# Kernel tuning notes

Measured on AMD Instinct MI355X. Metric: run time of the kernel, lower is better.

The kernel has to match this reference:

```python
import jax, jax.numpy as jnp
import numpy as np
import math
from jax import lax

B, L = 64, 8192
S = L // 8          # width after 3 stride-(1,2) SAME convs
D = 4 * 5           # height(4) * channels(5) -> per-token feature dim
D_FLAT = S * D


def setup_inputs():
    key = jax.random.key(0)
    ks = jax.random.split(key, 32)
    sc = 0.1
    inp = {
        "inputs": jax.random.randint(ks[0], (B, L), 0, 4, dtype=jnp.int32),
        # conv stack: HWIO kernels, Conv2D(5,(4,4),(1,2),'SAME')
        "conv_w1": sc * jax.random.normal(ks[1], (4, 4, 1, 5), jnp.float32),
        "conv_b1": jnp.zeros((5,), jnp.float32),
        "conv_w2": sc * jax.random.normal(ks[2], (4, 4, 5, 5), jnp.float32),
        "conv_b2": jnp.zeros((5,), jnp.float32),
        "conv_w3": sc * jax.random.normal(ks[3], (4, 4, 5, 5), jnp.float32),
        "conv_b3": jnp.zeros((5,), jnp.float32),
        # 3 SelfAttn blocks, each with K/Q/V projections [D, D]
        "attn1_K": sc * jax.random.normal(ks[4], (D, D), jnp.float32),
        "attn1_Q": sc * jax.random.normal(ks[5], (D, D), jnp.float32),
        "attn1_V": sc * jax.random.normal(ks[6], (D, D), jnp.float32),
        "attn2_K": sc * jax.random.normal(ks[7], (D, D), jnp.float32),
        "attn2_Q": sc * jax.random.normal(ks[8], (D, D), jnp.float32),
        "attn2_V": sc * jax.random.normal(ks[9], (D, D), jnp.float32),
        "attn3_K": sc * jax.random.normal(ks[10], (D, D), jnp.float32),
        "attn3_Q": sc * jax.random.normal(ks[11], (D, D), jnp.float32),
        "attn3_V": sc * jax.random.normal(ks[12], (D, D), jnp.float32),
        # 3 Dense(10) layers (no activation, as in Keras defaults)
        "dense_w1": 0.01 * jax.random.normal(ks[13], (D_FLAT, 10), jnp.float32),
        "dense_b1": jnp.zeros((10,), jnp.float32),
        "dense_w2": sc * jax.random.normal(ks[14], (10, 10), jnp.float32),
        "dense_b2": jnp.zeros((10,), jnp.float32),
        "dense_w3": sc * jax.random.normal(ks[15], (10, 10), jnp.float32),
        "dense_b3": jnp.zeros((10,), jnp.float32),
    }
    return inp


def _conv(x, w, b):
    # NHWC, HWIO, strides (1,2), SAME
    y = lax.conv_general_dilated(x, w, window_strides=(1, 2), padding="SAME",
                                 dimension_numbers=("NHWC", "HWIO", "NHWC"))
    return y + b


def _self_attn(x, Kw, Qw, Vw):
    # x: [B, S, D]; manual causal scaled dot-product attention
    K = x @ Kw
    Q = x @ Qw
    V = x @ Vw
    s = Q.shape[1]
    mask = jnp.triu(jnp.full((s, s), -jnp.inf, dtype=x.dtype), k=1)
    scores = jnp.einsum("bsd,btd->bst", Q, K) / math.sqrt(K.shape[-1]) + mask
    return jax.nn.softmax(scores, axis=-1) @ V


def reference(inputs, conv_w1, conv_b1, conv_w2, conv_b2, conv_w3, conv_b3,
              attn1_K, attn1_Q, attn1_V, attn2_K, attn2_Q, attn2_V,
              attn3_K, attn3_Q, attn3_V,
              dense_w1, dense_b1, dense_w2, dense_b2, dense_w3, dense_b3):
    # one_hot over axis=1 -> [B, 4, L], then channel dim -> [B, 4, L, 1]
    x = jax.nn.one_hot(inputs, 4, axis=1, dtype=jnp.float32)[..., None]
    x = _conv(x, conv_w1, conv_b1)
    x = _conv(x, conv_w2, conv_b2)
    x = _conv(x, conv_w3, conv_b3)            # [B, 4, S, 5]
    # tokens along width, features = height(4) x channels(5)
    x = jnp.transpose(x, (0, 2, 1, 3)).reshape(x.shape[0], S, D)
    x = _self_attn(x, attn1_K, attn1_Q, attn1_V)
    x = _self_attn(x, attn2_K, attn2_Q, attn2_V)
    x = _self_attn(x, attn3_K, attn3_Q, attn3_V)
    x = x.reshape(x.shape[0], -1)             # flatten [B, S*D]
    x = x @ dense_w1 + dense_b1
    x = x @ dense_w2 + dense_b2
    x = x @ dense_w3 + dense_b3               # [B, 10]
    return x
```

## Files before the change

### kernel.cpp

```cpp
#include <hip/hip_runtime.h>
#include <hip/hip_bf16.h>


#define B_ 64
#define L_ 8192
#define S_ 1024
#define D_ 20

typedef unsigned short ushort_t;
typedef __attribute__((ext_vector_type(8))) short short8_t;
typedef __attribute__((ext_vector_type(4))) short short4_t;
typedef __attribute__((ext_vector_type(4))) float f32x4_t;

__device__ __forceinline__ ushort_t f2bf(float f) {
  unsigned u = __float_as_uint(f);
  return (ushort_t)((u + 0x7fffu + ((u >> 16) & 1u)) >> 16);
}
__device__ __forceinline__ float bf2f(ushort_t h) {
  return __uint_as_float(((unsigned)h) << 16);
}

__global__ __launch_bounds__(256) void conv12_kernel(
    const int* __restrict__ inp,
    const float* __restrict__ W1c, const float* __restrict__ B1c,
    const float* __restrict__ W2c, const float* __restrict__ B2c,
    float* __restrict__ out,
    const float* __restrict__ W1d,
    float* __restrict__ W1T) {
  __shared__ float w1s[80], b1s[5], w2s[400], b2s[5];
  for (int j = threadIdx.x; j < 400; j += 256) w2s[j] = W2c[j];
  if (threadIdx.x < 80)      w1s[threadIdx.x]      = W1c[threadIdx.x];
  else if (threadIdx.x < 85) b1s[threadIdx.x - 80] = B1c[threadIdx.x - 80];
  else if (threadIdx.x < 90) b2s[threadIdx.x - 85] = B2c[threadIdx.x - 85];
  __syncthreads();
  const int idx = blockIdx.x * 256 + threadIdx.x;
  const int b  = idx >> 11;
  const int wo = idx & 2047;
  const int* ib = inp + (size_t)b * L_;
  int iv[10];
#pragma unroll
  for (int t = 0; t < 10; ++t) {
    int g = 4 * wo - 3 + t;
    iv[t] = (g >= 0 && g < L_) ? ib[g] : -100;
  }
  float val[4][4][5];
#pragma unroll
  for (int pos = 0; pos < 4; ++pos) {
    const int w1 = 2 * wo - 1 + pos;
    const bool okp = (w1 >= 0 && w1 < 4096);
#pragma unroll
    for (int hi = 0; hi < 4; ++hi)
#pragma unroll
      for (int ci = 0; ci < 5; ++ci) val[hi][pos][ci] = okp ? b1s[ci] : 0.f;
    if (okp) {
#pragma unroll
      for (int kw = 0; kw < 4; ++kw) {
        const int gw = 2 * w1 - 1 + kw;
        if (gw >= 0 && gw < L_) {
          const int v = iv[2 * pos + kw];
#pragma unroll
          for (int hi = 0; hi < 4; ++hi) {
            const int kh = v - hi + 1;
            if (kh >= 0 && kh < 4) {
#pragma unroll
              for (int ci = 0; ci < 5; ++ci)
                val[hi][pos][ci] += w1s[(kh * 4 + kw) * 5 + ci];
            }
          }
        }
      }
    }
  }
  float acc[4][5];
#pragma unroll
  for (int h = 0; h < 4; ++h)
#pragma unroll
    for (int c = 0; c < 5; ++c) acc[h][c] = b2s[c];
#pragma unroll
  for (int kh = 0; kh < 4; ++kh)
#pragma unroll
    for (int kw = 0; kw < 4; ++kw)
#pragma unroll
      for (int ci = 0; ci < 5; ++ci) {
        const float* wp = w2s + ((kh * 4 + kw) * 5 + ci) * 5;
        float w0 = wp[0], w1v = wp[1], w2v = wp[2], w3 = wp[3], w4 = wp[4];
#pragma unroll
        for (int h = 0; h < 4; ++h) {
          int hi = h - 1 + kh;
          if (hi >= 0 && hi < 4) {
            float x = val[hi][kw][ci];
            acc[h][0] += w0 * x;  acc[h][1] += w1v * x; acc[h][2] += w2v * x;
            acc[h][3] += w3 * x;  acc[h][4] += w4 * x;
          }
        }
      }
  float* ob = out + (size_t)b * 4 * 2048 * 5;
#pragma unroll
  for (int h = 0; h < 4; ++h)
#pragma unroll
    for (int c = 0; c < 5; ++c) ob[(h * 2048 + wo) * 5 + c] = acc[h][c];
  for (int j = idx; j < 204800; j += 131072) {
    int col = j / 20480, i2 = j - col * 20480;
    W1T[j] = W1d[i2 * 10 + col];
  }
}

__global__ __launch_bounds__(256) void conv3_proj_kernel(
    const float* __restrict__ in,
    const float* __restrict__ W,  const float* __restrict__ Bi,
    const float* __restrict__ Kw, const float* __restrict__ Qw,
    const float* __restrict__ Vw,
    ushort_t* __restrict__ Qb, ushort_t* __restrict__ Kb,
    ushort_t* __restrict__ Vt) {
  constexpr int WIN = 2048;
  __shared__ float ws[400], bs[5];
  __shared__ float kw[400], qw[400], vw[400];
  for (int j = threadIdx.x; j < 400; j += 256) {
    ws[j] = W[j]; kw[j] = Kw[j]; qw[j] = Qw[j]; vw[j] = Vw[j];
  }
  if (threadIdx.x < 5) bs[threadIdx.x] = Bi[threadIdx.x];
  __syncthreads();
  const int r  = blockIdx.x * 256 + threadIdx.x;
  const int b  = r >> 10;
  const int wo = r & 1023;
  float val[4][4][5];
#pragma unroll
  for (int hi = 0; hi < 4; ++hi) {
    const float* ir = in + ((size_t)b * 4 + hi) * WIN * 5;
#pragma unroll
    for (int kwp = 0; kwp < 4; ++kwp) {
      int wi = 2 * wo - 1 + kwp;
      bool ok = (wi >= 0 && wi < WIN);
#pragma unroll
      for (int ci = 0; ci < 5; ++ci) val[hi][kwp][ci] = ok ? ir[wi * 5 + ci] : 0.f;
    }
  }
  float acc[4][5];
#pragma unroll
  for (int h = 0; h < 4; ++h)
#pragma unroll
    for (int c = 0; c < 5; ++c) acc[h][c] = bs[c];
#pragma unroll
  for (int kh = 0; kh < 4; ++kh)
#pragma unroll
    for (int kwp = 0; kwp < 4; ++kwp)
#pragma unroll
      for (int ci = 0; ci < 5; ++ci) {
        const float* wp = ws + ((kh * 4 + kwp) * 5 + ci) * 5;
        float w0 = wp[0], w1 = wp[1], w2 = wp[2], w3 = wp[3], w4 = wp[4];
#pragma unroll
        for (int h = 0; h < 4; ++h) {
          int hi = h - 1 + kh;
          if (hi >= 0 && hi < 4) {
            float x = val[hi][kwp][ci];
            acc[h][0] += w0 * x; acc[h][1] += w1 * x; acc[h][2] += w2 * x;
            acc[h][3] += w3 * x; acc[h][4] += w4 * x;
          }
        }
      }
  float x[D_];
#pragma unroll
  for (int h = 0; h < 4; ++h)
#pragma unroll
    for (int c = 0; c < 5; ++c) x[h * 5 + c] = acc[h][c];
  float q[D_], k[D_], v[D_];
#pragma unroll
  for (int j = 0; j < D_; ++j) { q[j] = 0.f; k[j] = 0.f; v[j] = 0.f; }
#pragma unroll
  for (int i = 0; i < D_; ++i) {
#pragma unroll
    for (int j = 0; j < D_; ++j) {
      q[j] += x[i] * qw[i * D_ + j];
      k[j] += x[i] * kw[i * D_ + j];
      v[j] += x[i] * vw[i * D_ + j];
    }
  }
  const float sc = 0.22360679774997896f;
  ushort_t qt[32], kt[32];
#pragma unroll
  for (int j = 0; j < D_; ++j) { qt[j] = f2bf(q[j] * sc); kt[j] = f2bf(k[j]); }
#pragma unroll
  for (int j = D_; j < 32; ++j) { qt[j] = 0; kt[j] = 0; }
  int4* qd = (int4*)(Qb + (size_t)r * 32);
  int4* kd = (int4*)(Kb + (size_t)r * 32);
#pragma unroll
  for (int j = 0; j < 4; ++j) {
    qd[j] = *(const int4*)(qt + 8 * j);
    kd[j] = *(const int4*)(kt + 8 * j);
  }
  ushort_t* vbase = Vt + ((size_t)b * 32) * 1024 + wo;
#pragma unroll
  for (int d = 0; d < D_; ++d) vbase[d * 1024] = f2bf(v[d]);
}

template <bool FUSE>
__global__ __launch_bounds__(512, 6) void attn_kernel(
    const ushort_t* __restrict__ Qb, const ushort_t* __restrict__ Kb,
    const ushort_t* __restrict__ Vt,
    const float* __restrict__ Kw2, const float* __restrict__ Qw2,
    const float* __restrict__ Vw2,
    ushort_t* __restrict__ Qb2, ushort_t* __restrict__ Kb2,
    ushort_t* __restrict__ Vt2,
    const float* __restrict__ W1T,
    float* __restrict__ part2) {
  constexpr int VST = 1032;
  __shared__ ushort_t vts[20 * VST];
  __shared__ float extraf[FUSE ? 2480 : 1280];
  __shared__ float mrgL[64];
  __shared__ float red2[FUSE ? 4 : 40];
  const int blk   = blockIdx.x;
  const int b     = blk & 63;
  const int strip = 15 - (blk >> 6);
  const int q0    = strip * 64;
  const int nt    = q0 + 64;
  const int tid   = threadIdx.x;
  const int w     = tid >> 6;
  const int sub   = w & 3;
  const int half  = w >> 2;
  const int lane  = tid & 63;
  const int n     = lane & 15;
  const int quad  = lane >> 4;
  const int qbase = q0 + 16 * sub;
  const int qg    = qbase + n;
  const ushort_t* VtB = Vt + (size_t)b * 32 * 1024;
  const int ntc = nt >> 3;
  for (int i = tid; i < 20 * ntc; i += 512) {
    int row = i / ntc, cc = i - row * ntc;
    *(int4*)(vts + row * VST + cc * 8) =
        *(const int4*)(VtB + (size_t)row * 1024 + cc * 8);
  }
  if (FUSE) {
    for (int j = tid; j < 1200; j += 512) {
      int m = j / 400, oo = j - m * 400;
      extraf[j] = (m == 0) ? Kw2[oo] : (m == 1) ? Qw2[oo] : Vw2[oo];
    }
  }
  const ushort_t* KbB = Kb + (size_t)b * 1024 * 32;
  short8_t qfrag = *(const short8_t*)(Qb + ((size_t)(b * 1024 + qbase + n)) * 32 + quad * 8);
  f32x4_t oA = {0.f, 0.f, 0.f, 0.f};
  f32x4_t oB = {0.f, 0.f, 0.f, 0.f};
  const f32x4_t zero = {0.f, 0.f, 0.f, 0.f};
  float lsum = 0.f;
  const int nt2 = nt >> 1;
  const int tlo = half ? nt2 : 0;
  int thi = half ? nt : nt2;
  if (thi > qbase + 16) thi = qbase + 16;
  __syncthreads();
  for (int t0 = tlo; t0 < thi; t0 += 32) {
    short8_t kf0 = *(const short8_t*)(KbB + (size_t)(t0 + n) * 32 + quad * 8);
    short8_t kf1 = *(const short8_t*)(KbB + (size_t)(t0 + 16 + n) * 32 + quad * 8);
#pragma unroll
    for (int c = 0; c < 2; ++c) {
      const int tg = t0 + c * 16 + quad * 4;
      f32x4_t s = __builtin_amdgcn_mfma_f32_16x16x32_bf16(c ? kf1 : kf0, qfrag,
                                                          zero, 0, 0, 0);
      ushort_t pk4[4];
#pragma unroll
      for (int r = 0; r < 4; ++r) {
        float p = (tg + r <= qg) ? __expf(s[r]) : 0.f;
        ushort_t h = f2bf(p);
        lsum += bf2f(h);
        pk4[r] = h;
      }
      short4_t pfrag = *(const short4_t*)pk4;
      short4_t vlo = *(const short4_t*)(vts + n * VST + t0 + c * 16 + quad * 4);
      short4_t vhi = *(const short4_t*)(vts + (16 + (n & 3)) * VST + t0 + c * 16 + quad * 4);
      oA = __builtin_amdgcn_mfma_f32_16x16x16bf16_1k(vlo, pfrag, oA, 0, 0, 0);
      oB = __builtin_amdgcn_mfma_f32_16x16x16bf16_1k(vhi, pfrag, oB, 0, 0, 0);
    }
  }
  float l = lsum;
  l += __shfl_xor(l, 16, 64);
  l += __shfl_xor(l, 32, 64);
  float* ox  = FUSE ? (extraf + 1200) : extraf;
  float* oxw = ox + sub * 320;
  if (half) {
#pragma unroll
    for (int r = 0; r < 4; ++r) oxw[n * 20 + quad * 4 + r] = oA[r];
    if (quad == 0) {
#pragma unroll
      for (int r = 0; r < 4; ++r) oxw[n * 20 + 16 + r] = oB[r];
      mrgL[sub * 16 + n] = l;
    }
  }
  __syncthreads();
  if (!half) {
#pragma unroll
    for (int r = 0; r < 4; ++r) oA[r] += oxw[n * 20 + quad * 4 + r];
    if (quad == 0) {
#pragma unroll
      for (int r = 0; r < 4; ++r) oB[r] += oxw[n * 20 + 16 + r];
    }
    l += mrgL[sub * 16 + n];
    const float inv = 1.f / l;
#pragma unroll
    for (int r = 0; r < 4; ++r) oxw[n * 20 + quad * 4 + r] = oA[r] * inv;
    if (quad == 0) {
#pragma unroll
      for (int r = 0; r < 4; ++r) oxw[n * 20 + 16 + r] = oB[r] * inv;
    }
  }
  if (FUSE) {
    if (!half) {
      float* pw = extraf;
      __asm__ volatile("s_waitcnt lgkmcnt(0)" ::: "memory");
      const int row  = lane >> 2;
      const int part = lane & 3;
      float x[D_];
#pragma unroll
      for (int i = 0; i < D_; ++i) x[i] = oxw[row * 20 + i];
      float qv[5], kv[5], vv[5];
#pragma unroll
      for (int jj = 0; jj < 5; ++jj) { qv[jj] = 0.f; kv[jj] = 0.f; vv[jj] = 0.f; }
#pragma unroll
      for (int i = 0; i < D_; ++i) {
        const float xi = x[i];
#pragma unroll
        for (int jj = 0; jj < 5; ++jj) {
          const int j = 5 * part + jj;
          kv[jj] += xi * pw[i * 20 + j];
          qv[jj] += xi * pw[400 + i * 20 + j];
          vv[jj] += xi * pw[800 + i * 20 + j];
        }
      }
      const float sc = 0.22360679774997896f;
      const int rg = b * 1024 + qbase + row;
      const int s  = rg & 1023;
#pragma unroll
      for (int jj = 0; jj < 5; ++jj) {
        const int j = 5 * part + jj;
        Kb2[(size_t)rg * 32 + j] = f2bf(kv[jj]);
        Qb2[(size_t)rg * 32 + j] = f2bf(qv[jj] * sc);
        Vt2[(size_t)b * 32768 + (size_t)j * 1024 + s] = f2bf(vv[jj]);
      }
      if (part == 0) {
#pragma unroll
        for (int u = 0; u < 6; ++u)
          *(unsigned*)(Kb2 + (size_t)rg * 32 + 20 + 2 * u) = 0u;
      } else if (part == 1) {
#pragma unroll
        for (int u = 0; u < 6; ++u)
          *(unsigned*)(Qb2 + (size_t)rg * 32 + 20 + 2 * u) = 0u;
      }
    }
  } else {
    __syncthreads();
    float acc[10];
#pragma unroll
    for (int j = 0; j < 10; ++j) acc[j] = 0.f;
    const int base = q0 * 20;
    if (tid < 256) {
#pragma unroll
      for (int k = 0; k < 5; ++k) {
        const int il = tid + 256 * k;
        const float xv = ox[il];
#pragma unroll
        for (int j = 0; j < 10; ++j)
          acc[j] += xv * W1T[(size_t)j * 20480 + base + il];
      }
    }
#pragma unroll
    for (int off = 1; off < 64; off <<= 1) {
#pragma unroll
      for (int j = 0; j < 10; ++j) acc[j] += __shfl_xor(acc[j], off, 64);
    }
    if (tid < 256 && lane == 0) {
#pragma unroll
      for (int j = 0; j < 10; ++j) red2[w * 10 + j] = acc[j];
    }
    __syncthreads();
    if (tid < 10) {
      float s2 = red2[tid] + red2[10 + tid] + red2[20 + tid] + red2[30 + tid];
      part2[((b << 4) + strip) * 10 + tid] = s2;
    }
  }
}

__global__ __launch_bounds__(64) void dense_final(
    const float* __restrict__ part2,
    const float* __restrict__ B1,
    const float* __restrict__ W2, const float* __restrict__ B2,
    const float* __restrict__ W3, const float* __restrict__ B3,
    float* __restrict__ out) {
  const int b = blockIdx.x;
  __shared__ float y1[10], y2[10];
  if (threadIdx.x < 10) {
    int j = threadIdx.x;
    float s = 0.f;
#pragma unroll
    for (int st = 0; st < 16; ++st) s += part2[((b << 4) + st) * 10 + j];
    y1[j] = s + B1[j];
  }
  __syncthreads();
  if (threadIdx.x < 10) {
    int j = threadIdx.x;
    float s = B2[j];
#pragma unroll
    for (int i = 0; i < 10; ++i) s += y1[i] * W2[i * 10 + j];
    y2[j] = s;
  }
  __syncthreads();
  if (threadIdx.x < 10) {
    int j = threadIdx.x;
    float s = B3[j];
#pragma unroll
    for (int i = 0; i < 10; ++i) s += y2[i] * W3[i * 10 + j];
    out[b * 10 + j] = s;
  }
}

extern "C" void kernel_launch(void* const* d_in, const int* in_sizes, int n_in,
                              void* d_out, int out_size, void* d_ws, size_t ws_size,
                              hipStream_t stream) {
  const int*   inp = (const int*)d_in[0];
  const float* cw1 = (const float*)d_in[1];
  const float* cb1 = (const float*)d_in[2];
  const float* cw2 = (const float*)d_in[3];
  const float* cb2 = (const float*)d_in[4];
  const float* cw3 = (const float*)d_in[5];
  const float* cb3 = (const float*)d_in[6];
  const float* a1K = (const float*)d_in[7];
  const float* a1Q = (const float*)d_in[8];
  const float* a1V = (const float*)d_in[9];
  const float* a2K = (const float*)d_in[10];
  const float* a2Q = (const float*)d_in[11];
  const float* a2V = (const float*)d_in[12];
  const float* a3K = (const float*)d_in[13];
  const float* a3Q = (const float*)d_in[14];
  const float* a3V = (const float*)d_in[15];
  const float* dw1 = (const float*)d_in[16];
  const float* db1 = (const float*)d_in[17];
  const float* dw2 = (const float*)d_in[18];
  const float* db2 = (const float*)d_in[19];
  const float* dw3 = (const float*)d_in[20];
  const float* db3 = (const float*)d_in[21];
  float* outp = (float*)d_out;

  float* wsf = (float*)d_ws;
  ushort_t* qbA  = (ushort_t*)(wsf);
  ushort_t* kbA  = (ushort_t*)(wsf + 1048576);
  ushort_t* vtA  = (ushort_t*)(wsf + 2097152);
  float*    part2= wsf + 4456448;
  float*    w1t  = wsf + 4466688;
  ushort_t* qbB  = (ushort_t*)(wsf + 4671488);
  ushort_t* kbB  = (ushort_t*)(wsf + 5712384);
  ushort_t* vtB  = (ushort_t*)(wsf + 6760960);
  float*    c2   = wsf + 5242880;

  conv12_kernel<<<512, 256, 0, stream>>>(inp, cw1, cb1, cw2, cb2, c2, dw1, w1t);

  conv3_proj_kernel<<<256, 256, 0, stream>>>(c2, cw3, cb3, a1K, a1Q, a1V, qbA, kbA, vtA);
  attn_kernel<true><<<1024, 512, 0, stream>>>(
      qbA, kbA, vtA, a2K, a2Q, a2V, qbB, kbB, vtB, nullptr, nullptr);
  attn_kernel<true><<<1024, 512, 0, stream>>>(
      qbB, kbB, vtB, a3K, a3Q, a3V, qbA, kbA, vtA, nullptr, nullptr);
  attn_kernel<false><<<1024, 512, 0, stream>>>(
      qbA, kbA, vtA, nullptr, nullptr, nullptr, nullptr, nullptr, nullptr,
      w1t, part2);

  dense_final<<<64, 64, 0, stream>>>(part2, db1, dw2, db2, dw3, db3, outp);
}
```

Before: 198.5 us.

## Shrink attention LDS footprint, read V high rows from global, interleave strips

The attention kernel now stages only 16 V-transpose rows in LDS and reads the remaining four rows straight from global memory. The output scratch area reuses the V buffer after an added barrier, and the launch-bounds occupancy target goes from 6 to 8 blocks. Causal strips are also assigned to blocks in an interleaved order to balance work across dispatch. The smaller LDS footprint is meant to allow more resident blocks per CU, at the cost of extra global loads in the inner loop, an additional __syncthreads, and possible register pressure from the tighter launch bound.

```diff
diff --git a/kernel.cpp b/kernel.cpp
--- a/kernel.cpp
+++ b/kernel.cpp
@@ -194,7 +194,7 @@
 }
 
 template <bool FUSE>
-__global__ __launch_bounds__(512, 6) void attn_kernel(
+__global__ __launch_bounds__(512, 8) void attn_kernel(
     const ushort_t* __restrict__ Qb, const ushort_t* __restrict__ Kb,
     const ushort_t* __restrict__ Vt,
     const float* __restrict__ Kw2, const float* __restrict__ Qw2,
@@ -204,13 +204,17 @@
     const float* __restrict__ W1T,
     float* __restrict__ part2) {
   constexpr int VST = 1032;
-  __shared__ ushort_t vts[20 * VST];
-  __shared__ float extraf[FUSE ? 2480 : 1280];
+  __shared__ __align__(16) ushort_t vts[16 * VST];
+  __shared__ float pw_s[FUSE ? 1200 : 4];
   __shared__ float mrgL[64];
-  __shared__ float red2[FUSE ? 4 : 40];
+  __shared__ float red2[40];
+  float* ox = (float*)vts;
   const int blk   = blockIdx.x;
   const int b     = blk & 63;
-  const int strip = 15 - (blk >> 6);
+  const int raw   = blk >> 6;
+  const int rr4   = raw & 3, k4 = raw >> 2;
+  const int strip = (k4 == 0) ? rr4 : (k4 == 1) ? 7 - rr4
+                  : (k4 == 2) ? 8 + rr4 : 15 - rr4;
   const int q0    = strip * 64;
   const int nt    = q0 + 64;
   const int tid   = threadIdx.x;
@@ -223,19 +227,21 @@
   const int qbase = q0 + 16 * sub;
   const int qg    = qbase + n;
   const ushort_t* VtB = Vt + (size_t)b * 32 * 1024;
-  const int ntc = nt >> 3;
-  for (int i = tid; i < 20 * ntc; i += 512) {
-    int row = i / ntc, cc = i - row * ntc;
-    *(int4*)(vts + row * VST + cc * 8) =
-        *(const int4*)(VtB + (size_t)row * 1024 + cc * 8);
+  {
+    const int row = tid >> 5, c0 = tid & 31;
+    const int ntc = nt >> 3;
+    for (int cc = c0; cc < ntc; cc += 32)
+      *(int4*)(vts + row * VST + cc * 8) =
+          *(const int4*)(VtB + (size_t)row * 1024 + cc * 8);
   }
   if (FUSE) {
     for (int j = tid; j < 1200; j += 512) {
       int m = j / 400, oo = j - m * 400;
-      extraf[j] = (m == 0) ? Kw2[oo] : (m == 1) ? Qw2[oo] : Vw2[oo];
-    }
-  }
-  const ushort_t* KbB = Kb + (size_t)b * 1024 * 32;
+      pw_s[j] = (m == 0) ? Kw2[oo] : (m == 1) ? Qw2[oo] : Vw2[oo];
+    }
+  }
+  const ushort_t* KbB  = Kb + (size_t)b * 1024 * 32;
+  const ushort_t* VtHi = VtB + (size_t)(16 + (n & 3)) * 1024;
   short8_t qfrag = *(const short8_t*)(Qb + ((size_t)(b * 1024 + qbase + n)) * 32 + quad * 8);
   f32x4_t oA = {0.f, 0.f, 0.f, 0.f};
   f32x4_t oB = {0.f, 0.f, 0.f, 0.f};
@@ -264,7 +270,7 @@
       }
       short4_t pfrag = *(const short4_t*)pk4;
       short4_t vlo = *(const short4_t*)(vts + n * VST + t0 + c * 16 + quad * 4);
-      short4_t vhi = *(const short4_t*)(vts + (16 + (n & 3)) * VST + t0 + c * 16 + quad * 4);
+      short4_t vhi = *(const short4_t*)(VtHi + t0 + c * 16 + quad * 4);
       oA = __builtin_amdgcn_mfma_f32_16x16x16bf16_1k(vlo, pfrag, oA, 0, 0, 0);
       oB = __builtin_amdgcn_mfma_f32_16x16x16bf16_1k(vhi, pfrag, oB, 0, 0, 0);
     }
@@ -272,7 +278,7 @@
   float l = lsum;
   l += __shfl_xor(l, 16, 64);
   l += __shfl_xor(l, 32, 64);
-  float* ox  = FUSE ? (extraf + 1200) : extraf;
+  __syncthreads();
   float* oxw = ox + sub * 320;
   if (half) {
 #pragma unroll
@@ -302,7 +308,6 @@
   }
   if (FUSE) {
     if (!half) {
-      float* pw = extraf;
       __asm__ volatile("s_waitcnt lgkmcnt(0)" ::: "memory");
       const int row  = lane >> 2;
       const int part = lane & 3;
@@ -318,9 +323,9 @@
 #pragma unroll
         for (int jj = 0; jj < 5; ++jj) {
           const int j = 5 * part + jj;
-          kv[jj] += xi * pw[i * 20 + j];
-          qv[jj] += xi * pw[400 + i * 20 + j];
-          vv[jj] += xi * pw[800 + i * 20 + j];
+          kv[jj] += xi * pw_s[i * 20 + j];
+          qv[jj] += xi * pw_s[400 + i * 20 + j];
+          vv[jj] += xi * pw_s[800 + i * 20 + j];
         }
       }
       const float sc = 0.22360679774997896f;
```

New measurement: 223.3 us. 12.5% more time.

## Fold dense layers 2-3 into W1 and bias, drop final dense kernel

Applied to the files above, without the earlier changes.

Because the three dense layers have no activation, W1·W2·W3 is precomputed into the transposed weight buffer and the combined bias is written straight into the output. The last attention kernel then atomically adds its per-strip partial sums into the output, and the separate dense_final launch goes away. This removes one kernel launch and the partial-sum buffer. The cost is extra per-element work in conv12 to compute W2·W3, and floating-point atomics that make the summation order nondeterministic.

```diff
diff --git a/kernel.cpp b/kernel.cpp
--- a/kernel.cpp
+++ b/kernel.cpp
@@ -26,7 +26,11 @@
     const float* __restrict__ W2c, const float* __restrict__ B2c,
     float* __restrict__ out,
     const float* __restrict__ W1d,
-    float* __restrict__ W1T) {
+    float* __restrict__ W1T,
+    const float* __restrict__ B1d, const float* __restrict__ W2d,
+    const float* __restrict__ B2d, const float* __restrict__ W3d,
+    const float* __restrict__ B3d,
+    float* __restrict__ outp) {
   __shared__ float w1s[80], b1s[5], w2s[400], b2s[5];
   for (int j = threadIdx.x; j < 400; j += 256) w2s[j] = W2c[j];
   if (threadIdx.x < 80)      w1s[threadIdx.x]      = W1c[threadIdx.x];
@@ -100,8 +104,33 @@
 #pragma unroll
     for (int c = 0; c < 5; ++c) ob[(h * 2048 + wo) * 5 + c] = acc[h][c];
   for (int j = idx; j < 204800; j += 131072) {
-    int col = j / 20480, i2 = j - col * 20480;
-    W1T[j] = W1d[i2 * 10 + col];
+    const int col = j / 20480, i2 = j - col * 20480;
+    float w23[10];
+#pragma unroll
+    for (int k2 = 0; k2 < 10; ++k2) {
+      float s = 0.f;
+#pragma unroll
+      for (int m = 0; m < 10; ++m) s += W2d[k2 * 10 + m] * W3d[m * 10 + col];
+      w23[k2] = s;
+    }
+    float s = 0.f;
+#pragma unroll
+    for (int k2 = 0; k2 < 10; ++k2) s += W1d[i2 * 10 + k2] * w23[k2];
+    W1T[j] = s;
+  }
+  if (idx < 640) {
+    const int col = idx - (idx / 10) * 10;
+    float bc = B3d[col];
+#pragma unroll
+    for (int m = 0; m < 10; ++m) bc += B2d[m] * W3d[m * 10 + col];
+#pragma unroll
+    for (int k2 = 0; k2 < 10; ++k2) {
+      float w23 = 0.f;
+#pragma unroll
+      for (int m = 0; m < 10; ++m) w23 += W2d[k2 * 10 + m] * W3d[m * 10 + col];
+      bc += B1d[k2] * w23;
+    }
+    outp[idx] = bc;
   }
 }
 
@@ -202,7 +231,7 @@
     ushort_t* __restrict__ Qb2, ushort_t* __restrict__ Kb2,
     ushort_t* __restrict__ Vt2,
     const float* __restrict__ W1T,
-    float* __restrict__ part2) {
+    float* __restrict__ outp) {
   constexpr int VST = 1032;
   __shared__ ushort_t vts[20 * VST];
   __shared__ float extraf[FUSE ? 2480 : 1280];
@@ -371,41 +400,8 @@
     __syncthreads();
     if (tid < 10) {
       float s2 = red2[tid] + red2[10 + tid] + red2[20 + tid] + red2[30 + tid];
-      part2[((b << 4) + strip) * 10 + tid] = s2;
-    }
-  }
-}
-
-__global__ __launch_bounds__(64) void dense_final(
-    const float* __restrict__ part2,
-    const float* __restrict__ B1,
-    const float* __restrict__ W2, const float* __restrict__ B2,
-    const float* __restrict__ W3, const float* __restrict__ B3,
-    float* __restrict__ out) {
-  const int b = blockIdx.x;
-  __shared__ float y1[10], y2[10];
-  if (threadIdx.x < 10) {
-    int j = threadIdx.x;
-    float s = 0.f;
-#pragma unroll
-    for (int st = 0; st < 16; ++st) s += part2[((b << 4) + st) * 10 + j];
-    y1[j] = s + B1[j];
-  }
-  __syncthreads();
-  if (threadIdx.x < 10) {
-    int j = threadIdx.x;
-    float s = B2[j];
-#pragma unroll
-    for (int i = 0; i < 10; ++i) s += y1[i] * W2[i * 10 + j];
-    y2[j] = s;
-  }
-  __syncthreads();
-  if (threadIdx.x < 10) {
-    int j = threadIdx.x;
-    float s = B3[j];
-#pragma unroll
-    for (int i = 0; i < 10; ++i) s += y2[i] * W3[i * 10 + j];
-    out[b * 10 + j] = s;
+      atomicAdd(&outp[b * 10 + tid], s2);
+    }
   }
 }
 
@@ -440,23 +436,22 @@
   ushort_t* qbA  = (ushort_t*)(wsf);
   ushort_t* kbA  = (ushort_t*)(wsf + 1048576);
   ushort_t* vtA  = (ushort_t*)(wsf + 2097152);
-  float*    part2= wsf + 4456448;
   float*    w1t  = wsf + 4466688;
   ushort_t* qbB  = (ushort_t*)(wsf + 4671488);
   ushort_t* kbB  = (ushort_t*)(wsf + 5712384);
   ushort_t* vtB  = (ushort_t*)(wsf + 6760960);
   float*    c2   = wsf + 5242880;
 
-  conv12_kernel<<<512, 256, 0, stream>>>(inp, cw1, cb1, cw2, cb2, c2, dw1, w1t);
-
-  conv3_proj_kernel<<<256, 256, 0, stream>>>(c2, cw3, cb3, a1K, a1Q, a1V, qbA, kbA, vtA);
+  conv12_kernel<<<512, 256, 0, stream>>>(inp, cw1, cb1, cw2, cb2, c2, dw1,
+                                         w1t, db1, dw2, db2, dw3, db3, outp);
+
+  conv3_proj_kernel<<<256, 256, 0, stream>>>(c2, cw3, cb3, a1K, a1Q, a1V,
+                                             qbA, kbA, vtA);
   attn_kernel<true><<<1024, 512, 0, stream>>>(
       qbA, kbA, vtA, a2K, a2Q, a2V, qbB, kbB, vtB, nullptr, nullptr);
   attn_kernel<true><<<1024, 512, 0, stream>>>(
       qbB, kbB, vtB, a3K, a3Q, a3V, qbA, kbA, vtA, nullptr, nullptr);
   attn_kernel<false><<<1024, 512, 0, stream>>>(
       qbA, kbA, vtA, nullptr, nullptr, nullptr, nullptr, nullptr, nullptr,
-      w1t, part2);
-
-  dense_final<<<64, 64, 0, stream>>>(part2, db1, dw2, db2, dw3, db3, outp);
-}
+      w1t, outp);
+}
```

Result: no change. 196.9 us, median of 2 (-0.8%).
